# Optimization experiments

Hardware: AMD Instinct MI355X
Metric: run time of the kernel (lower is better)

The kernel has to match this reference:

```python
import jax, jax.numpy as jnp
import numpy as np

B, S, D, H, E, TOPK = 8, 1024, 512, 2048, 8, 2


def setup_inputs() -> dict:
    key = jax.random.key(0)
    ks = jax.random.split(key, 7)
    scale = 0.02
    return {
        "x": jax.random.normal(ks[0], (B, S, D), jnp.float32),
        "gate_w": jax.random.normal(ks[1], (D, E), jnp.float32) * scale,
        "gate_b": jnp.zeros((E,), jnp.float32),
        "w1": jax.random.normal(ks[2], (E, D, H), jnp.float32) * scale,
        "b1": jnp.zeros((E, H), jnp.float32),
        "w2": jax.random.normal(ks[3], (E, H, D), jnp.float32) * scale,
        "b2": jnp.zeros((E, D), jnp.float32),
    }


def reference(x, gate_w, gate_b, w1, b1, w2, b2):
    # ---- MoE transformer MLP (fastmoe FMoETransformerMLP, NaiveGate) ----
    xt = x.reshape(-1, D)                       # [T, D], T = B*S tokens
    logits = xt @ gate_w + gate_b               # [T, E]
    top_val, top_idx = jax.lax.top_k(logits, TOPK)  # [T, k]
    score = jax.nn.softmax(top_val, axis=-1)    # softmax over the k selected logits

    y = jnp.zeros_like(xt)
    # Loop over the small fixed expert set; each token's combine weight for
    # expert e is the sum of its top-k scores routed to e (0 if not selected).
    for e in range(E):
        w_tok = jnp.sum(score * (top_idx == e), axis=-1)        # [T]
        h = jax.nn.gelu(xt @ w1[e] + b1[e], approximate=False)  # [T, H]
        y = y + w_tok[:, None] * (h @ w2[e] + b2[e])            # [T, D]

    y = y.reshape(B, S, D)
    # Outer model: log_softmax over seq of channel-summed features
    return jax.nn.log_softmax(jnp.sum(y, axis=2), axis=1)       # [B, S]
```

## Files before the change

kernel.cpp:

```cpp
#include <hip/hip_runtime.h>
#include <hip/hip_bf16.h>
#include <math.h>

#define T_TOK 8192
#define DIM   512
#define NEXP  8
#define HID   2048
#define NBAT  8
#define SEQ   1024

typedef short  short8 __attribute__((ext_vector_type(8)));
typedef float  f32x4  __attribute__((ext_vector_type(4)));

__device__ __forceinline__ unsigned short f2bf(float f) {
    union { float f; unsigned int u; } v; v.f = f;
    unsigned int u = v.u;
    unsigned int r = u + 0x7FFFu + ((u >> 16) & 1u);
    return (unsigned short)(r >> 16);
}

__device__ __forceinline__ float gelu_f(float v) {
    float v2 = v * v;
    float w = v * (-2.302344f - 0.102955f * v2);
    return v / (1.f + __builtin_amdgcn_exp2f(w));
}

__global__ void prep_k(const float* __restrict__ x, const float* __restrict__ gw,
                       const float* __restrict__ gb, unsigned short* __restrict__ xb,
                       int* __restrict__ eidx, float* __restrict__ esc0,
                       float* __restrict__ esc1,
                       const float* __restrict__ w1, unsigned short* __restrict__ w1t,
                       const float* __restrict__ w2, const float* __restrict__ b2,
                       float* __restrict__ w2sum, float* __restrict__ b2sum,
                       int* __restrict__ counts) {
    int bid = blockIdx.x;
    int tid = threadIdx.x;
    int wave = tid >> 6, lane = tid & 63;
    if (bid < 2048) {
        int t = bid * 4 + wave;
        const float* xp = x + (size_t)t * DIM + lane * 8;
        float4 xa = *(const float4*)(xp);
        float4 xc = *(const float4*)(xp + 4);
        unsigned short pk8[8];
        pk8[0] = f2bf(xa.x); pk8[1] = f2bf(xa.y); pk8[2] = f2bf(xa.z); pk8[3] = f2bf(xa.w);
        pk8[4] = f2bf(xc.x); pk8[5] = f2bf(xc.y); pk8[6] = f2bf(xc.z); pk8[7] = f2bf(xc.w);
        *(short8*)(xb + (size_t)t * DIM + lane * 8) = *(short8*)pk8;
        float acc[8] = {0, 0, 0, 0, 0, 0, 0, 0};
        const float* gwp = gw + lane * 8 * 8;
        float xv[8] = {xa.x, xa.y, xa.z, xa.w, xc.x, xc.y, xc.z, xc.w};
        #pragma unroll
        for (int j = 0; j < 8; ++j) {
            float4 g0 = *(const float4*)(gwp + j * 8);
            float4 g1 = *(const float4*)(gwp + j * 8 + 4);
            acc[0] += xv[j] * g0.x; acc[1] += xv[j] * g0.y;
            acc[2] += xv[j] * g0.z; acc[3] += xv[j] * g0.w;
            acc[4] += xv[j] * g1.x; acc[5] += xv[j] * g1.y;
            acc[6] += xv[j] * g1.z; acc[7] += xv[j] * g1.w;
        }
        #pragma unroll
        for (int e = 0; e < 8; ++e) {
            float s = acc[e];
            #pragma unroll
            for (int off = 32; off >= 1; off >>= 1) s += __shfl_xor(s, off);
            acc[e] = s + gb[e];
        }
        float v0 = -1e30f, v1 = -1e30f; int i0 = 0, i1 = 0;
        #pragma unroll
        for (int e = 0; e < 8; ++e) {
            float v = acc[e];
            if (v > v0) { v1 = v0; i1 = i0; v0 = v; i0 = e; }
            else if (v > v1) { v1 = v; i1 = e; }
        }
        float e1 = expf(v1 - v0);
        float inv = 1.f / (1.f + e1);
        if (lane == 0) {
            eidx[t] = i0 | (i1 << 4);
            esc0[t] = inv;
            esc1[t] = e1 * inv;
        }
    } else if (bid < 4096) {
        __shared__ unsigned short tile[64][65];
        int r = bid - 2048;
        int e = r >> 8; r &= 255;
        int d0 = (r & 7) * 64, h0 = (r >> 3) * 64;
        const float* src = w1 + (size_t)e * DIM * HID;
        #pragma unroll
        for (int pass = 0; pass < 4; ++pass) {
            int dr = pass * 16 + (tid >> 4);
            int hc = (tid & 15) * 4;
            float4 v = *(const float4*)(src + (size_t)(d0 + dr) * HID + h0 + hc);
            tile[hc + 0][dr] = f2bf(v.x);
            tile[hc + 1][dr] = f2bf(v.y);
            tile[hc + 2][dr] = f2bf(v.z);
            tile[hc + 3][dr] = f2bf(v.w);
        }
        __syncthreads();
        unsigned short* dst = w1t + (size_t)e * HID * DIM;
        #pragma unroll
        for (int pass = 0; pass < 4; ++pass) {
            int hr = pass * 16 + (tid >> 4);
            int dc = (tid & 15) * 4;
            ushort4 o;
            o.x = tile[hr][dc];     o.y = tile[hr][dc + 1];
            o.z = tile[hr][dc + 2]; o.w = tile[hr][dc + 3];
            *(ushort4*)(dst + (size_t)(h0 + hr) * DIM + d0 + dc) = o;
        }
    } else if (bid < 8192) {
        int row = (bid - 4096) * 4 + wave;
        const float* p = w2 + (size_t)row * DIM;
        float4 a = *(const float4*)(p + lane * 4);
        float4 b = *(const float4*)(p + 256 + lane * 4);
        float s = a.x + a.y + a.z + a.w + b.x + b.y + b.z + b.w;
        #pragma unroll
        for (int off = 32; off >= 1; off >>= 1) s += __shfl_xor(s, off);
        if (lane == 0) w2sum[row] = s;
    } else {
        if (tid < 8) counts[tid] = 0;
        for (int r = wave; r < NEXP; r += 4) {
            const float* p = b2 + (size_t)r * DIM;
            float s = 0.f;
            for (int i = lane; i < DIM; i += 64) s += p[i];
            #pragma unroll
            for (int off = 32; off >= 1; off >>= 1) s += __shfl_xor(s, off);
            if (lane == 0) b2sum[r] = s;
        }
    }
}

__global__ __launch_bounds__(1024) void route_k(
    const int* __restrict__ eidx, const float* __restrict__ esc0,
    const float* __restrict__ esc1, const float* __restrict__ b2sum,
    int* __restrict__ counts, int* __restrict__ ptok, float* __restrict__ pscore,
    float* __restrict__ s_partial) {
    int tid = threadIdx.x;
    int t = blockIdx.x * 1024 + tid;
    int wv = tid >> 6, lane = tid & 63;
    int pk = eidx[t];
    int i0 = pk & 0xf, i1 = (pk >> 4) & 0xf;
    float s0 = esc0[t], s1 = esc1[t];
    s_partial[t] = s0 * b2sum[i0] + s1 * b2sum[i1];

    __shared__ int waveCnt[16][8];
    __shared__ int waveBase[16][8];

    unsigned long long m0[8], m1[8];
    #pragma unroll
    for (int e = 0; e < 8; ++e) {
        m0[e] = __ballot(i0 == e);
        m1[e] = __ballot(i1 == e);
    }
    if (lane < 8) {
        int c = 0;
        #pragma unroll
        for (int e = 0; e < 8; ++e)
            if (lane == e) c = __popcll(m0[e]) + __popcll(m1[e]);
        waveCnt[wv][lane] = c;
    }
    __syncthreads();
    if (tid < 8) {
        int e = tid;
        int total = 0;
        #pragma unroll
        for (int w = 0; w < 16; ++w) total += waveCnt[w][e];
        int base = atomicAdd(&counts[e], total);
        int run = base;
        #pragma unroll
        for (int w = 0; w < 16; ++w) {
            waveBase[w][e] = run;
            run += waveCnt[w][e];
        }
    }
    __syncthreads();

    unsigned long long lt = (1ULL << lane) - 1ULL;
    int slot0 = 0, slot1 = 0;
    #pragma unroll
    for (int e = 0; e < 8; ++e) {
        if (i0 == e) slot0 = waveBase[wv][e] + __popcll(m0[e] & lt);
        if (i1 == e) slot1 = waveBase[wv][e] + __popcll(m0[e]) + __popcll(m1[e] & lt);
    }
    ptok[i0 * T_TOK + slot0] = t;  pscore[i0 * T_TOK + slot0] = s0;
    ptok[i1 * T_TOK + slot1] = t;  pscore[i1 * T_TOK + slot1] = s1;
}

#define GPTR(p) (const __attribute__((address_space(1))) void*)(p)
#define LPTR(p) (__attribute__((address_space(3))) void*)(p)

__global__ __launch_bounds__(256) void moe_gemm_k(
    const unsigned short* __restrict__ xb, const unsigned short* __restrict__ w1t,
    const float* __restrict__ b1, const float* __restrict__ w2sum,
    const int* __restrict__ counts, const int* __restrict__ ptok,
    const float* __restrict__ pscore, float* __restrict__ s_partial) {

    int bx = blockIdx.x;
    int e = 8, rowBase = 0, accT = 0;
    #pragma unroll
    for (int i = 0; i < 8; ++i) {
        int nt = (counts[i] + 127) >> 7;
        if (e == 8 && bx < accT + nt) { e = i; rowBase = (bx - accT) * 128; }
        accT += nt;
    }
    if (e == 8) return;
    int n_e = counts[e];
    int hBase = blockIdx.y * 128;

    __shared__ unsigned short A_s[128 * 64];
    __shared__ unsigned short B_s[128 * 64];
    __shared__ int   tokLds[128];
    __shared__ float scoreLds[128];

    int tid = threadIdx.x;
    int wave = tid >> 6, lane = tid & 63;

    if (tid < 128) {
        int r = rowBase + tid;
        bool valid = r < n_e;
        tokLds[tid]   = valid ? ptok[e * T_TOK + r]   : 0;
        scoreLds[tid] = valid ? pscore[e * T_TOK + r] : 0.f;
    }
    switch ((bx + blockIdx.y) & 3) {
        case 1: __builtin_amdgcn_s_sleep(2); break;
        case 2: __builtin_amdgcn_s_sleep(4); break;
        case 3: __builtin_amdgcn_s_sleep(6); break;
        default: break;
    }
    __syncthreads();

    const unsigned short* gA[4];
    const unsigned short* gB[4];
    int lo[4];
    #pragma unroll
    for (int i = 0; i < 4; ++i) {
        int c = (i * 4 + wave) * 64 + lane;
        int row = c >> 3, pos = c & 7;
        int j = (pos ^ (row & 7)) * 8;
        gA[i] = xb + (size_t)tokLds[row] * DIM + j;
        gB[i] = w1t + ((size_t)e * HID + hBase + row) * DIM + j;
        lo[i] = c * 8;
    }

    int wm = wave >> 1, wn = wave & 1;
    int quad = lane >> 4, col = lane & 15;

    f32x4 acc[4][4];
    #pragma unroll
    for (int m = 0; m < 4; ++m)
        #pragma unroll
        for (int n = 0; n < 4; ++n)
            acc[m][n] = (f32x4){0.f, 0.f, 0.f, 0.f};

    for (int kk = 0; kk < 8; ++kk) {
        __syncthreads();
        int ko = ((kk + bx) & 7) * 64;
        #pragma unroll
        for (int i = 0; i < 4; ++i) {
            __builtin_amdgcn_global_load_lds(GPTR(gA[i] + ko), LPTR(&A_s[lo[i]]), 16, 0, 0);
            __builtin_amdgcn_global_load_lds(GPTR(gB[i] + ko), LPTR(&B_s[lo[i]]), 16, 0, 0);
        }
        __syncthreads();
        __builtin_amdgcn_s_setprio(1);
        #pragma unroll
        for (int kh = 0; kh < 2; ++kh) {
            int swz = (((kh << 2) | quad) ^ (col & 7)) * 8;
            const unsigned short* aB = A_s + (wm * 64 + col) * 64 + swz;
            const unsigned short* bB = B_s + (wn * 64 + col) * 64 + swz;
            short8 af[4], bf[4];
            #pragma unroll
            for (int m = 0; m < 4; ++m) af[m] = *(const short8*)(aB + m * 16 * 64);
            #pragma unroll
            for (int n = 0; n < 4; ++n) bf[n] = *(const short8*)(bB + n * 16 * 64);
            #pragma unroll
            for (int m = 0; m < 4; ++m)
                #pragma unroll
                for (int n = 0; n < 4; ++n)
                    acc[m][n] = __builtin_amdgcn_mfma_f32_16x16x32_bf16(af[m], bf[n], acc[m][n], 0, 0, 0);
        }
        __builtin_amdgcn_s_setprio(0);
    }

    const float* b1e = b1 + e * HID;
    const float* w2e = w2sum + e * HID;
    float bias[4], wsum[4];
    #pragma unroll
    for (int n = 0; n < 4; ++n) {
        int h = hBase + wn * 64 + n * 16 + col;
        bias[n] = b1e[h];
        wsum[n] = w2e[h];
    }
    #pragma unroll
    for (int m = 0; m < 4; ++m) {
        float rp0 = 0.f, rp1 = 0.f, rp2 = 0.f, rp3 = 0.f;
        #pragma unroll
        for (int n = 0; n < 4; ++n) {
            rp0 += gelu_f(acc[m][n][0] + bias[n]) * wsum[n];
            rp1 += gelu_f(acc[m][n][1] + bias[n]) * wsum[n];
            rp2 += gelu_f(acc[m][n][2] + bias[n]) * wsum[n];
            rp3 += gelu_f(acc[m][n][3] + bias[n]) * wsum[n];
        }
        #pragma unroll
        for (int off = 8; off >= 1; off >>= 1) {
            rp0 += __shfl_xor(rp0, off);
            rp1 += __shfl_xor(rp1, off);
            rp2 += __shfl_xor(rp2, off);
            rp3 += __shfl_xor(rp3, off);
        }
        if (col < 4) {
            float mine = (col == 0) ? rp0 : (col == 1) ? rp1 : (col == 2) ? rp2 : rp3;
            int rl = wm * 64 + m * 16 + quad * 4 + col;
            int r = rowBase + rl;
            if (r < n_e)
                atomicAdd(&s_partial[tokLds[rl]], scoreLds[rl] * mine);
        }
    }
}

__global__ void lsm_k(const float* __restrict__ s, float* __restrict__ out) {
    int b = blockIdx.x, tid = threadIdx.x;
    int wave = tid >> 6, lane = tid & 63;
    __shared__ float red[4];
    const float* sp = s + (size_t)b * SEQ;
    float v[4];
    #pragma unroll
    for (int i = 0; i < 4; ++i) v[i] = sp[tid + i * 256];
    float m = fmaxf(fmaxf(v[0], v[1]), fmaxf(v[2], v[3]));
    #pragma unroll
    for (int off = 32; off >= 1; off >>= 1) m = fmaxf(m, __shfl_xor(m, off));
    if (lane == 0) red[wave] = m;
    __syncthreads();
    m = fmaxf(fmaxf(red[0], red[1]), fmaxf(red[2], red[3]));
    __syncthreads();
    float t = 0.f;
    #pragma unroll
    for (int i = 0; i < 4; ++i) t += expf(v[i] - m);
    #pragma unroll
    for (int off = 32; off >= 1; off >>= 1) t += __shfl_xor(t, off);
    if (lane == 0) red[wave] = t;
    __syncthreads();
    t = red[0] + red[1] + red[2] + red[3];
    float L = m + logf(t);
    #pragma unroll
    for (int i = 0; i < 4; ++i) out[(size_t)b * SEQ + tid + i * 256] = v[i] - L;
}

extern "C" void kernel_launch(void* const* d_in, const int* in_sizes, int n_in,
                              void* d_out, int out_size, void* d_ws, size_t ws_size,
                              hipStream_t stream) {
    const float* x  = (const float*)d_in[0];
    const float* gw = (const float*)d_in[1];
    const float* gb = (const float*)d_in[2];
    const float* w1 = (const float*)d_in[3];
    const float* b1 = (const float*)d_in[4];
    const float* w2 = (const float*)d_in[5];
    const float* b2 = (const float*)d_in[6];
    float* out = (float*)d_out;

    char* ws = (char*)d_ws;
    int*   counts    = (int*)  (ws + 0);
    float* b2sum     = (float*)(ws + 1280);
    float* s_partial = (float*)(ws + 1536);
    float* w2sum     = (float*)(ws + 34304);
    int*   ptok      = (int*)  (ws + 99840);
    float* pscore    = (float*)(ws + 361984);
    int*   eidx      = (int*)  (ws + 624128);
    float* esc0      = (float*)(ws + 656896);
    float* esc1      = (float*)(ws + 689664);
    unsigned short* xb  = (unsigned short*)(ws + 722432);
    unsigned short* w1t = (unsigned short*)(ws + 9111040);

    prep_k<<<8193, 256, 0, stream>>>(x, gw, gb, xb, eidx, esc0, esc1,
                                     w1, w1t, w2, b2, w2sum, b2sum, counts);
    route_k<<<NEXP, 1024, 0, stream>>>(eidx, esc0, esc1, b2sum, counts, ptok, pscore, s_partial);
    moe_gemm_k<<<dim3(135, 16), 256, 0, stream>>>(xb, w1t, b1, w2sum, counts, ptok, pscore, s_partial);
    lsm_k<<<NBAT, 256, 0, stream>>>(s_partial, out);
}
```

Before: 214.3 us.

## Prefetch next K-tile into registers to overlap global loads with MFMA

Replaces direct global-to-LDS loads with a register-staged software pipeline. Each iteration stores the prefetched registers to LDS, syncs with a lighter lgkmcnt wait plus barrier, and then issues the global loads for the next K-slice before running the MFMAs. This is meant to hide global memory latency behind compute. The cost is extra VGPRs for the staging buffers and explicit ds_write instructions, which could reduce occupancy.

```diff
diff --git a/kernel.cpp b/kernel.cpp
--- a/kernel.cpp
+++ b/kernel.cpp
@@ -23,6 +23,11 @@
     float v2 = v * v;
     float w = v * (-2.302344f - 0.102955f * v2);
     return v / (1.f + __builtin_amdgcn_exp2f(w));
+}
+
+__device__ __forceinline__ void sync_lds() {
+    asm volatile("s_waitcnt lgkmcnt(0)" ::: "memory");
+    __builtin_amdgcn_s_barrier();
 }
 
 __global__ void prep_k(const float* __restrict__ x, const float* __restrict__ gw,
@@ -183,9 +188,6 @@
     ptok[i1 * T_TOK + slot1] = t;  pscore[i1 * T_TOK + slot1] = s1;
 }
 
-#define GPTR(p) (const __attribute__((address_space(1))) void*)(p)
-#define LPTR(p) (__attribute__((address_space(3))) void*)(p)
-
 __global__ __launch_bounds__(256) void moe_gemm_k(
     const unsigned short* __restrict__ xb, const unsigned short* __restrict__ w1t,
     const float* __restrict__ b1, const float* __restrict__ w2sum,
@@ -228,7 +230,8 @@
 
     const unsigned short* gA[4];
     const unsigned short* gB[4];
-    int lo[4];
+    unsigned short* lA[4];
+    unsigned short* lB[4];
     #pragma unroll
     for (int i = 0; i < 4; ++i) {
         int c = (i * 4 + wave) * 64 + lane;
@@ -236,7 +239,8 @@
         int j = (pos ^ (row & 7)) * 8;
         gA[i] = xb + (size_t)tokLds[row] * DIM + j;
         gB[i] = w1t + ((size_t)e * HID + hBase + row) * DIM + j;
-        lo[i] = c * 8;
+        lA[i] = &A_s[c * 8];
+        lB[i] = &B_s[c * 8];
     }
 
     int wm = wave >> 1, wn = wave & 1;
@@ -249,15 +253,32 @@
         for (int n = 0; n < 4; ++n)
             acc[m][n] = (f32x4){0.f, 0.f, 0.f, 0.f};
 
+    int4 rA[4], rB[4];
+    {
+        int ko = (bx & 7) * 64;
+        #pragma unroll
+        for (int i = 0; i < 4; ++i) {
+            rA[i] = *(const int4*)(gA[i] + ko);
+            rB[i] = *(const int4*)(gB[i] + ko);
+        }
+    }
+
     for (int kk = 0; kk < 8; ++kk) {
-        __syncthreads();
-        int ko = ((kk + bx) & 7) * 64;
+        sync_lds();
         #pragma unroll
         for (int i = 0; i < 4; ++i) {
-            __builtin_amdgcn_global_load_lds(GPTR(gA[i] + ko), LPTR(&A_s[lo[i]]), 16, 0, 0);
-            __builtin_amdgcn_global_load_lds(GPTR(gB[i] + ko), LPTR(&B_s[lo[i]]), 16, 0, 0);
-        }
-        __syncthreads();
+            *(int4*)lA[i] = rA[i];
+            *(int4*)lB[i] = rB[i];
+        }
+        sync_lds();
+        if (kk < 7) {
+            int ko = ((kk + 1 + bx) & 7) * 64;
+            #pragma unroll
+            for (int i = 0; i < 4; ++i) {
+                rA[i] = *(const int4*)(gA[i] + ko);
+                rB[i] = *(const int4*)(gB[i] + ko);
+            }
+        }
         __builtin_amdgcn_s_setprio(1);
         #pragma unroll
         for (int kh = 0; kh < 2; ++kh) {
```

After: 319.8 us. +49.3%, slower.

## Load expert weight fragments directly from global instead of staging through LDS

Applied to the files above, without the earlier changes.

The B operand (w1t weight tile) is no longer copied into shared memory; each wave reads its MFMA B fragments straight from global memory into registers, which halves LDS use per block. The first barrier becomes a lighter lgkmcnt wait plus s_barrier, and launch bounds now request 4 blocks per CU for higher occupancy. This removes LDS staging traffic and one set of LDS reads for B. In exchange, global loads now sit on the MFMA critical path with no prefetch, and the two column-half waves sharing a B slice each fetch it separately.

```diff
diff --git a/kernel.cpp b/kernel.cpp
--- a/kernel.cpp
+++ b/kernel.cpp
@@ -23,6 +23,11 @@
     float v2 = v * v;
     float w = v * (-2.302344f - 0.102955f * v2);
     return v / (1.f + __builtin_amdgcn_exp2f(w));
+}
+
+__device__ __forceinline__ void sync_lds() {
+    asm volatile("s_waitcnt lgkmcnt(0)" ::: "memory");
+    __builtin_amdgcn_s_barrier();
 }
 
 __global__ void prep_k(const float* __restrict__ x, const float* __restrict__ gw,
@@ -186,7 +191,7 @@
 #define GPTR(p) (const __attribute__((address_space(1))) void*)(p)
 #define LPTR(p) (__attribute__((address_space(3))) void*)(p)
 
-__global__ __launch_bounds__(256) void moe_gemm_k(
+__global__ __launch_bounds__(256, 4) void moe_gemm_k(
     const unsigned short* __restrict__ xb, const unsigned short* __restrict__ w1t,
     const float* __restrict__ b1, const float* __restrict__ w2sum,
     const int* __restrict__ counts, const int* __restrict__ ptok,
@@ -205,7 +210,6 @@
     int hBase = blockIdx.y * 128;
 
     __shared__ unsigned short A_s[128 * 64];
-    __shared__ unsigned short B_s[128 * 64];
     __shared__ int   tokLds[128];
     __shared__ float scoreLds[128];
 
@@ -227,21 +231,22 @@
     __syncthreads();
 
     const unsigned short* gA[4];
-    const unsigned short* gB[4];
-    int lo[4];
+    int loA[4];
     #pragma unroll
     for (int i = 0; i < 4; ++i) {
         int c = (i * 4 + wave) * 64 + lane;
         int row = c >> 3, pos = c & 7;
         int j = (pos ^ (row & 7)) * 8;
         gA[i] = xb + (size_t)tokLds[row] * DIM + j;
-        gB[i] = w1t + ((size_t)e * HID + hBase + row) * DIM + j;
-        lo[i] = c * 8;
+        loA[i] = c * 8;
     }
 
     int wm = wave >> 1, wn = wave & 1;
     int quad = lane >> 4, col = lane & 15;
 
+    const unsigned short* bBase =
+        w1t + ((size_t)e * HID + hBase + wn * 64 + col) * DIM + quad * 8;
+
     f32x4 acc[4][4];
     #pragma unroll
     for (int m = 0; m < 4; ++m)
@@ -250,30 +255,28 @@
             acc[m][n] = (f32x4){0.f, 0.f, 0.f, 0.f};
 
     for (int kk = 0; kk < 8; ++kk) {
-        __syncthreads();
+        sync_lds();
         int ko = ((kk + bx) & 7) * 64;
         #pragma unroll
-        for (int i = 0; i < 4; ++i) {
-            __builtin_amdgcn_global_load_lds(GPTR(gA[i] + ko), LPTR(&A_s[lo[i]]), 16, 0, 0);
-            __builtin_amdgcn_global_load_lds(GPTR(gB[i] + ko), LPTR(&B_s[lo[i]]), 16, 0, 0);
-        }
+        for (int i = 0; i < 4; ++i)
+            __builtin_amdgcn_global_load_lds(GPTR(gA[i] + ko), LPTR(&A_s[loA[i]]), 16, 0, 0);
         __syncthreads();
         __builtin_amdgcn_s_setprio(1);
         #pragma unroll
         for (int kh = 0; kh < 2; ++kh) {
+            short8 bf[4];
+            #pragma unroll
+            for (int n = 0; n < 4; ++n)
+                bf[n] = *(const short8*)(bBase + (size_t)n * 16 * DIM + ko + kh * 32);
             int swz = (((kh << 2) | quad) ^ (col & 7)) * 8;
             const unsigned short* aB = A_s + (wm * 64 + col) * 64 + swz;
-            const unsigned short* bB = B_s + (wn * 64 + col) * 64 + swz;
-            short8 af[4], bf[4];
             #pragma unroll
-            for (int m = 0; m < 4; ++m) af[m] = *(const short8*)(aB + m * 16 * 64);
-            #pragma unroll
-            for (int n = 0; n < 4; ++n) bf[n] = *(const short8*)(bB + n * 16 * 64);
-            #pragma unroll
-            for (int m = 0; m < 4; ++m)
+            for (int m = 0; m < 4; ++m) {
+                short8 af = *(const short8*)(aB + m * 16 * 64);
                 #pragma unroll
                 for (int n = 0; n < 4; ++n)
-                    acc[m][n] = __builtin_amdgcn_mfma_f32_16x16x32_bf16(af[m], bf[n], acc[m][n], 0, 0, 0);
+                    acc[m][n] = __builtin_amdgcn_mfma_f32_16x16x32_bf16(af, bf[n], acc[m][n], 0, 0, 0);
+            }
         }
         __builtin_amdgcn_s_setprio(0);
     }
```

Result: slower. 233.2 us (+8.9%).
